# Optimization experiments

Measured on AMD Instinct MI355X. Metric: run time of the kernel, lower is better.

Reference implementation:

```python
import jax, jax.numpy as jnp
import numpy as np

BN_EPS = 1e-5  # torch BatchNorm1d default


def setup_inputs() -> dict:
    key = jax.random.key(0)
    k = jax.random.split(key, 5)
    B, D, L = 4096, 4096, 4  # batch, width, num layers (3 hidden + 1 output)
    x = jax.random.normal(k[0], (B, D), dtype=jnp.float32)
    # Per-layer Linear weights stored as [L, in, out]; scaled like xavier-ish init.
    W = jax.random.normal(k[1], (L, D, D), dtype=jnp.float32) * (1.0 / np.sqrt(D))
    b = jax.random.normal(k[2], (L, D), dtype=jnp.float32) * 0.01
    gamma = jax.random.uniform(k[3], (L, D), dtype=jnp.float32, minval=0.5, maxval=1.5)
    beta = jax.random.normal(k[4], (L, D), dtype=jnp.float32) * 0.1
    return {"x": x, "W": W, "b": b, "gamma": gamma, "beta": beta}


def _layer(h, W_l, b_l, gamma_l, beta_l):
    # one big GEMM replaces the per-neuron GEMV loop + stack
    h = h @ W_l + b_l  # [B, out]
    # BatchNorm1d, training mode: biased batch stats over the batch dim
    mu = jnp.mean(h, axis=0)
    var = jnp.var(h, axis=0)
    h = (h - mu) * jax.lax.rsqrt(var + BN_EPS) * gamma_l + beta_l
    return jax.nn.relu(h)


def reference(x, W, b, gamma, beta):
    out = x
    for l in range(W.shape[0]):  # small fixed layer count
        out = _layer(out, W[l], b[l], gamma[l], beta[l])
    # nn.Softmax(dim=0): softmax over the batch dimension, as in the original
    return jax.nn.softmax(out, axis=0)
```

## Files before the change

kernel.cpp:

```cpp
#include <hip/hip_runtime.h>
#include <stdint.h>

#define DIMD 4096
#define DIMB 4096
#define NLAYER 4
#define NT (DIMD / 64)

typedef unsigned short u16;
typedef __attribute__((ext_vector_type(4))) float f32x4;
typedef __attribute__((ext_vector_type(8))) __bf16 bf16x8;

__device__ __forceinline__ u16 f2bf(float f) {
    union { float f; uint32_t u; } v; v.f = f;
    return (u16)((v.u + 0x7fffu + ((v.u >> 16) & 1u)) >> 16);
}
__device__ __forceinline__ float bf2f(u16 u) {
    union { uint32_t u; float f; } v; v.u = ((uint32_t)u) << 16;
    return v.f;
}

__global__ void k_cvt(const float* __restrict__ in, u16* __restrict__ out) {
    int i = (blockIdx.x * 256 + threadIdx.x) * 4;
    float4 v = *reinterpret_cast<const float4*>(in + i);
    ushort4 r;
    r.x = f2bf(v.x); r.y = f2bf(v.y); r.z = f2bf(v.z); r.w = f2bf(v.w);
    *reinterpret_cast<ushort4*>(out + i) = r;
}

__global__ void k_trans(const float* __restrict__ W, u16* __restrict__ Wt) {
    __shared__ float tile[64][65];
    const int t = threadIdx.x;
    const size_t loff = (size_t)blockIdx.z * DIMD * DIMD;
    const int n0 = blockIdx.x * 64, k0 = blockIdx.y * 64;
    const int kr = t >> 4, c4 = (t & 15) * 4;
    #pragma unroll
    for (int r = 0; r < 4; ++r) {
        float4 v = *reinterpret_cast<const float4*>(W + loff + (size_t)(k0 + kr + r * 16) * DIMD + n0 + c4);
        tile[kr + r * 16][c4 + 0] = v.x;
        tile[kr + r * 16][c4 + 1] = v.y;
        tile[kr + r * 16][c4 + 2] = v.z;
        tile[kr + r * 16][c4 + 3] = v.w;
    }
    __syncthreads();
    const int nr = t >> 4, k4 = (t & 15) * 4;
    #pragma unroll
    for (int r = 0; r < 4; ++r) {
        int n = nr + r * 16;
        ushort4 o;
        o.x = f2bf(tile[k4 + 0][n]);
        o.y = f2bf(tile[k4 + 1][n]);
        o.z = f2bf(tile[k4 + 2][n]);
        o.w = f2bf(tile[k4 + 3][n]);
        *reinterpret_cast<ushort4*>(Wt + loff + (size_t)(n0 + n) * DIMD + k0 + k4) = o;
    }
}

#define GLD(g, l) __builtin_amdgcn_global_load_lds( \
    (__attribute__((address_space(1))) void*)(g),   \
    (__attribute__((address_space(3))) void*)(l), 16, 0, 0)

#define VMW8 asm volatile("s_waitcnt vmcnt(8)" ::: "memory")
#define VMW0 asm volatile("s_waitcnt vmcnt(0)" ::: "memory")
#define LGKM0 asm volatile("s_waitcnt lgkmcnt(0)" ::: "memory")

__global__ __launch_bounds__(512, 2) void k_gemm(
        const u16* __restrict__ A, const u16* __restrict__ Bt,
        const float* __restrict__ bias, u16* __restrict__ H,
        float* __restrict__ Hf,
        float* __restrict__ csum, float* __restrict__ csum2) {
    __shared__ __attribute__((aligned(16))) u16 As[2 * 256 * 64];
    __shared__ __attribute__((aligned(16))) u16 Bs[2 * 256 * 64];
    const int tid = threadIdx.x;
    const int lane = tid & 63, wv = tid >> 6;
    const int wm = wv >> 2, wn = wv & 3;
    const int bm = blockIdx.y, bn = blockIdx.x;
    const int lr = lane & 15, lk = lane >> 4;

    const int r0 = tid >> 3;
    const int cswz = (tid & 7) ^ (r0 & 7);
    const u16* gA = A  + (size_t)(bm * 256 + r0) * DIMD + cswz * 8;
    const u16* gB = Bt + (size_t)(bn * 256 + r0) * DIMD + cswz * 8;

#define STAGE_A(h, t, buf) do { \
    const u16* _s = gA + (size_t)(h) * 128 * DIMD + (size_t)(t) * 64; \
    u16* _d = As + (buf) * 16384 + (h) * 8192 + wv * 512; \
    GLD(_s, _d); GLD(_s + (size_t)64 * DIMD, _d + 4096); \
} while (0)
#define STAGE_B(h, t, buf) do { \
    const u16* _s = gB + (size_t)(h) * 128 * DIMD + (size_t)(t) * 64; \
    u16* _d = Bs + (buf) * 16384 + (h) * 8192 + wv * 512; \
    GLD(_s, _d); GLD(_s + (size_t)64 * DIMD, _d + 4096); \
} while (0)

    int aoff[4][2], boff[2][2];
    #pragma unroll
    for (int mf = 0; mf < 4; ++mf)
        #pragma unroll
        for (int ks = 0; ks < 2; ++ks) {
            int row = wm * 128 + mf * 16 + lr;
            aoff[mf][ks] = row * 64 + ((ks * 4 + lk) ^ (row & 7)) * 8;
        }
    #pragma unroll
    for (int nf = 0; nf < 2; ++nf)
        #pragma unroll
        for (int ks = 0; ks < 2; ++ks) {
            int row = wn * 64 + nf * 16 + lr;
            boff[nf][ks] = row * 64 + ((ks * 4 + lk) ^ (row & 7)) * 8;
        }

    f32x4 acc[8][4] = {};
    bf16x8 a[4][2], b0[2][2], b1[2][2];

#define READ_ALO(Ab) _Pragma("unroll") for (int mf = 0; mf < 4; ++mf) \
    _Pragma("unroll") for (int ks = 0; ks < 2; ++ks) \
        a[mf][ks] = *reinterpret_cast<const bf16x8*>((Ab) + aoff[mf][ks])
#define READ_AHI(Ab) _Pragma("unroll") for (int mf = 0; mf < 4; ++mf) \
    _Pragma("unroll") for (int ks = 0; ks < 2; ++ks) \
        a[mf][ks] = *reinterpret_cast<const bf16x8*>((Ab) + 4096 + aoff[mf][ks])
#define READ_B0(Bb) _Pragma("unroll") for (int nf = 0; nf < 2; ++nf) \
    _Pragma("unroll") for (int ks = 0; ks < 2; ++ks) \
        b0[nf][ks] = *reinterpret_cast<const bf16x8*>((Bb) + boff[nf][ks])
#define READ_B1(Bb) _Pragma("unroll") for (int nf = 0; nf < 2; ++nf) \
    _Pragma("unroll") for (int ks = 0; ks < 2; ++ks) \
        b1[nf][ks] = *reinterpret_cast<const bf16x8*>((Bb) + 2048 + boff[nf][ks])
#define MFMA_Q(MO, B, NO) _Pragma("unroll") for (int mf = 0; mf < 4; ++mf) \
    _Pragma("unroll") for (int nf = 0; nf < 2; ++nf) \
    _Pragma("unroll") for (int ks = 0; ks < 2; ++ks) \
        acc[(MO) + mf][(NO) + nf] = __builtin_amdgcn_mfma_f32_16x16x32_bf16( \
            a[mf][ks], B[nf][ks], acc[(MO) + mf][(NO) + nf], 0, 0, 0)

#define TILE(CUR, TN, PF, WEND) do { \
    const u16* Ab = As + (CUR) * 16384; \
    const u16* Bb = Bs + (CUR) * 16384; \
     \
    READ_ALO(Ab); READ_B0(Bb); \
    __builtin_amdgcn_s_barrier(); \
    LGKM0; \
    __builtin_amdgcn_s_setprio(1); \
    MFMA_Q(0, b0, 0); \
    __builtin_amdgcn_s_setprio(0); \
    __builtin_amdgcn_s_barrier(); \
     \
    READ_B1(Bb); \
    __builtin_amdgcn_s_barrier(); \
    LGKM0; \
    __builtin_amdgcn_s_setprio(1); \
    MFMA_Q(0, b1, 2); \
    __builtin_amdgcn_s_setprio(0); \
    __builtin_amdgcn_s_barrier(); \
     \
    READ_AHI(Ab); \
    if (PF) { STAGE_B(0, TN, CUR); STAGE_B(1, TN, CUR); } \
    __builtin_amdgcn_s_barrier(); \
    LGKM0; \
    __builtin_amdgcn_s_setprio(1); \
    MFMA_Q(4, b1, 2); \
    __builtin_amdgcn_s_setprio(0); \
    __builtin_amdgcn_s_barrier(); \
     \
    if (PF) { STAGE_A(0, TN, CUR); STAGE_A(1, TN, CUR); } \
    __builtin_amdgcn_s_setprio(1); \
    MFMA_Q(4, b0, 0); \
    __builtin_amdgcn_s_setprio(0); \
    WEND; \
    __builtin_amdgcn_s_barrier(); \
} while (0)

    STAGE_B(0, 0, 0); STAGE_B(1, 0, 0); STAGE_A(0, 0, 0); STAGE_A(1, 0, 0);
    STAGE_B(0, 1, 1); STAGE_B(1, 1, 1); STAGE_A(0, 1, 1); STAGE_A(1, 1, 1);
    VMW8;
    __builtin_amdgcn_s_barrier();

    for (int tt = 0; tt < NT - 2; tt += 2) {
        TILE(0, tt + 2, true, VMW8);
        TILE(1, tt + 3, true, VMW8);
    }
    TILE(0, 0, false, VMW0);
    TILE(1, 0, false, VMW0);

    #pragma unroll
    for (int nh = 0; nh < 2; ++nh)
        #pragma unroll
        for (int nf = 0; nf < 2; ++nf) {
            int n = nh * 2 + nf;
            int col = bn * 256 + wn * 64 + nh * 32 + nf * 16 + lr;
            float bv = bias[col];
            float s1 = 0.f, s2 = 0.f;
            #pragma unroll
            for (int m = 0; m < 8; ++m) {
                int rbase = bm * 256 + wm * 128 + (m >> 2) * 64 + (m & 3) * 16 + lk * 4;
                #pragma unroll
                for (int r = 0; r < 4; ++r) {
                    float v = acc[m][n][r] + bv;
                    if (Hf) Hf[(size_t)(rbase + r) * DIMD + col] = v;
                    else    H [(size_t)(rbase + r) * DIMD + col] = f2bf(v);
                    s1 += v; s2 += v * v;
                }
            }
            s1 += __shfl_xor(s1, 16); s1 += __shfl_xor(s1, 32);
            s2 += __shfl_xor(s2, 16); s2 += __shfl_xor(s2, 32);
            if (lk == 0) {
                atomicAdd(&csum[col], s1);
                atomicAdd(&csum2[col], s2);
            }
        }
#undef TILE
#undef STAGE_A
#undef STAGE_B
}

__global__ void k_norm(const u16* __restrict__ H, const float* __restrict__ sum,
                       const float* __restrict__ sum2, const float* __restrict__ gamma,
                       const float* __restrict__ beta, u16* __restrict__ o) {
    int j = (blockIdx.x * 256 + threadIdx.x) * 4;
    int i0 = blockIdx.y * 32;
    float4 sm = *reinterpret_cast<const float4*>(sum + j);
    float4 s2 = *reinterpret_cast<const float4*>(sum2 + j);
    float4 gm = *reinterpret_cast<const float4*>(gamma + j);
    float4 bt = *reinterpret_cast<const float4*>(beta + j);
    float s[4], tt[4];
    #pragma unroll
    for (int c = 0; c < 4; ++c) {
        float mu = (&sm.x)[c] * (1.0f / DIMB);
        float var = (&s2.x)[c] * (1.0f / DIMB) - mu * mu;
        s[c] = (&gm.x)[c] * rsqrtf(var + 1e-5f);
        tt[c] = (&bt.x)[c] - mu * s[c];
    }
    for (int i = i0; i < i0 + 32; ++i) {
        ushort4 h = *reinterpret_cast<const ushort4*>(H + (size_t)i * DIMD + j);
        ushort4 r;
        #pragma unroll
        for (int c = 0; c < 4; ++c)
            (&r.x)[c] = f2bf(fmaxf(bf2f((&h.x)[c]) * s[c] + tt[c], 0.0f));
        *reinterpret_cast<ushort4*>(o + (size_t)i * DIMD + j) = r;
    }
}

__global__ void k_esum(const float* __restrict__ H, const float* __restrict__ sum,
                       const float* __restrict__ sum2, const float* __restrict__ gamma,
                       const float* __restrict__ beta, float* __restrict__ esum) {
    int j = (blockIdx.x * 256 + threadIdx.x) * 4;
    int i0 = blockIdx.y * 32;
    float4 sm = *reinterpret_cast<const float4*>(sum + j);
    float4 s2 = *reinterpret_cast<const float4*>(sum2 + j);
    float4 gm = *reinterpret_cast<const float4*>(gamma + j);
    float4 bt = *reinterpret_cast<const float4*>(beta + j);
    float s[4], tt[4], acc[4] = {0.f, 0.f, 0.f, 0.f};
    #pragma unroll
    for (int c = 0; c < 4; ++c) {
        float mu = (&sm.x)[c] * (1.0f / DIMB);
        float var = (&s2.x)[c] * (1.0f / DIMB) - mu * mu;
        s[c] = (&gm.x)[c] * rsqrtf(var + 1e-5f);
        tt[c] = (&bt.x)[c] - mu * s[c];
    }
    for (int i = i0; i < i0 + 32; ++i) {
        float4 h = *reinterpret_cast<const float4*>(H + (size_t)i * DIMD + j);
        #pragma unroll
        for (int c = 0; c < 4; ++c)
            acc[c] += __expf(fmaxf((&h.x)[c] * s[c] + tt[c], 0.0f));
    }
    #pragma unroll
    for (int c = 0; c < 4; ++c) atomicAdd(&esum[j + c], acc[c]);
}

__global__ void k_final(float* __restrict__ H, const float* __restrict__ sum,
                        const float* __restrict__ sum2, const float* __restrict__ gamma,
                        const float* __restrict__ beta, const float* __restrict__ esum) {
    int j = (blockIdx.x * 256 + threadIdx.x) * 4;
    int i0 = blockIdx.y * 32;
    float4 sm = *reinterpret_cast<const float4*>(sum + j);
    float4 s2 = *reinterpret_cast<const float4*>(sum2 + j);
    float4 gm = *reinterpret_cast<const float4*>(gamma + j);
    float4 bt = *reinterpret_cast<const float4*>(beta + j);
    float4 es = *reinterpret_cast<const float4*>(esum + j);
    float s[4], tt[4], inv[4];
    #pragma unroll
    for (int c = 0; c < 4; ++c) {
        float mu = (&sm.x)[c] * (1.0f / DIMB);
        float var = (&s2.x)[c] * (1.0f / DIMB) - mu * mu;
        s[c] = (&gm.x)[c] * rsqrtf(var + 1e-5f);
        tt[c] = (&bt.x)[c] - mu * s[c];
        inv[c] = 1.0f / (&es.x)[c];
    }
    for (int i = i0; i < i0 + 32; ++i) {
        float4 h = *reinterpret_cast<const float4*>(H + (size_t)i * DIMD + j);
        float4 o;
        #pragma unroll
        for (int c = 0; c < 4; ++c)
            (&o.x)[c] = __expf(fmaxf((&h.x)[c] * s[c] + tt[c], 0.0f)) * inv[c];
        *reinterpret_cast<float4*>(H + (size_t)i * DIMD + j) = o;
    }
}

extern "C" void kernel_launch(void* const* d_in, const int* in_sizes, int n_in,
                              void* d_out, int out_size, void* d_ws, size_t ws_size,
                              hipStream_t stream) {
    (void)in_sizes; (void)n_in; (void)out_size; (void)ws_size;
    const float* x     = (const float*)d_in[0];
    const float* W     = (const float*)d_in[1];
    const float* b     = (const float*)d_in[2];
    const float* gamma = (const float*)d_in[3];
    const float* beta  = (const float*)d_in[4];
    float* out = (float*)d_out;

    char* ws = (char*)d_ws;
    u16*  Abf = (u16*)ws;
    u16*  Wt4 = (u16*)(ws + (size_t)32 * 1024 * 1024);
    u16*  Hbf = (u16*)(ws + (size_t)160 * 1024 * 1024);
    float* stats = (float*)(ws + (size_t)192 * 1024 * 1024);
    hipMemsetAsync(stats, 0, (4 * 8192 + 4096) * sizeof(float), stream);

    k_cvt<<<DIMB * DIMD / 1024, 256, 0, stream>>>(x, Abf);
    k_trans<<<dim3(64, 64, 4), 256, 0, stream>>>(W, Wt4);

    for (int l = 0; l < NLAYER; ++l) {
        float* sum = stats + l * 8192;
        float* sum2 = sum + 4096;
        float* Hf = (l == NLAYER - 1) ? out : nullptr;
        k_gemm<<<dim3(16, 16), 512, 0, stream>>>(Abf, Wt4 + (size_t)l * DIMD * DIMD,
                                                 b + l * DIMD, Hbf, Hf, sum, sum2);
        if (l < NLAYER - 1)
            k_norm<<<dim3(4, 128), 256, 0, stream>>>(Hbf, sum, sum2,
                gamma + l * DIMD, beta + l * DIMD, Abf);
    }
    k_esum<<<dim3(4, 128), 256, 0, stream>>>(out, stats + 3 * 8192, stats + 3 * 8192 + 4096,
        gamma + 3 * DIMD, beta + 3 * DIMD, stats + 32768);
    k_final<<<dim3(4, 128), 256, 0, stream>>>(out, stats + 3 * 8192, stats + 3 * 8192 + 4096,
        gamma + 3 * DIMD, beta + 3 * DIMD, stats + 32768);
}
```

Baseline: 708.0 us.

## Stage GEMM epilogue through LDS for coalesced vector stores; widen norm kernel

```diff
diff --git a/kernel.cpp b/kernel.cpp
--- a/kernel.cpp
+++ b/kernel.cpp
@@ -7,6 +7,7 @@
 #define NT (DIMD / 64)
 
 typedef unsigned short u16;
+typedef __attribute__((ext_vector_type(8))) unsigned short us8;
 typedef __attribute__((ext_vector_type(4))) float f32x4;
 typedef __attribute__((ext_vector_type(8))) __bf16 bf16x8;
 
@@ -132,7 +133,6 @@
 #define TILE(CUR, TN, PF, WEND) do { \
     const u16* Ab = As + (CUR) * 16384; \
     const u16* Bb = Bs + (CUR) * 16384; \
-     \
     READ_ALO(Ab); READ_B0(Bb); \
     __builtin_amdgcn_s_barrier(); \
     LGKM0; \
@@ -140,7 +140,6 @@
     MFMA_Q(0, b0, 0); \
     __builtin_amdgcn_s_setprio(0); \
     __builtin_amdgcn_s_barrier(); \
-     \
     READ_B1(Bb); \
     __builtin_amdgcn_s_barrier(); \
     LGKM0; \
@@ -148,7 +147,6 @@
     MFMA_Q(0, b1, 2); \
     __builtin_amdgcn_s_setprio(0); \
     __builtin_amdgcn_s_barrier(); \
-     \
     READ_AHI(Ab); \
     if (PF) { STAGE_B(0, TN, CUR); STAGE_B(1, TN, CUR); } \
     __builtin_amdgcn_s_barrier(); \
@@ -157,7 +155,6 @@
     MFMA_Q(4, b1, 2); \
     __builtin_amdgcn_s_setprio(0); \
     __builtin_amdgcn_s_barrier(); \
-     \
     if (PF) { STAGE_A(0, TN, CUR); STAGE_A(1, TN, CUR); } \
     __builtin_amdgcn_s_setprio(1); \
     MFMA_Q(4, b0, 0); \
@@ -183,20 +180,17 @@
         #pragma unroll
         for (int nf = 0; nf < 2; ++nf) {
             int n = nh * 2 + nf;
-            int col = bn * 256 + wn * 64 + nh * 32 + nf * 16 + lr;
+            int col = bn * 256 + wn * 64 + n * 16 + lr;
             float bv = bias[col];
             float s1 = 0.f, s2 = 0.f;
             #pragma unroll
-            for (int m = 0; m < 8; ++m) {
-                int rbase = bm * 256 + wm * 128 + (m >> 2) * 64 + (m & 3) * 16 + lk * 4;
+            for (int m = 0; m < 8; ++m)
                 #pragma unroll
                 for (int r = 0; r < 4; ++r) {
                     float v = acc[m][n][r] + bv;
-                    if (Hf) Hf[(size_t)(rbase + r) * DIMD + col] = v;
-                    else    H [(size_t)(rbase + r) * DIMD + col] = f2bf(v);
+                    acc[m][n][r] = v;
                     s1 += v; s2 += v * v;
                 }
-            }
             s1 += __shfl_xor(s1, 16); s1 += __shfl_xor(s1, 32);
             s2 += __shfl_xor(s2, 16); s2 += __shfl_xor(s2, 32);
             if (lk == 0) {
@@ -204,6 +198,38 @@
                 atomicAdd(&csum2[col], s2);
             }
         }
+
+    float* Ls = reinterpret_cast<float*>(As) + wv * 1088;
+    const int erow = lane >> 3, ecol = (lane & 7) * 8;
+    #pragma unroll
+    for (int mf = 0; mf < 8; ++mf) {
+        #pragma unroll
+        for (int n = 0; n < 4; ++n)
+            #pragma unroll
+            for (int r = 0; r < 4; ++r)
+                Ls[(lk * 4 + r) * 68 + n * 16 + lr] = acc[mf][n][r];
+        LGKM0;
+        #pragma unroll
+        for (int g = 0; g < 2; ++g) {
+            int rowloc = erow + g * 8;
+            size_t gidx = (size_t)(bm * 256 + wm * 128 + mf * 16 + rowloc) * DIMD
+                        + bn * 256 + wn * 64 + ecol;
+            const float* src = Ls + rowloc * 68 + ecol;
+            if (Hf) {
+                float4 v0, v1;
+                v0.x = src[0]; v0.y = src[1]; v0.z = src[2]; v0.w = src[3];
+                v1.x = src[4]; v1.y = src[5]; v1.z = src[6]; v1.w = src[7];
+                *reinterpret_cast<float4*>(Hf + gidx) = v0;
+                *reinterpret_cast<float4*>(Hf + gidx + 4) = v1;
+            } else {
+                us8 o;
+                #pragma unroll
+                for (int c = 0; c < 8; ++c) o[c] = f2bf(src[c]);
+                *reinterpret_cast<us8*>(H + gidx) = o;
+            }
+        }
+        LGKM0;
+    }
 #undef TILE
 #undef STAGE_A
 #undef STAGE_B
@@ -212,27 +238,30 @@
 __global__ void k_norm(const u16* __restrict__ H, const float* __restrict__ sum,
                        const float* __restrict__ sum2, const float* __restrict__ gamma,
                        const float* __restrict__ beta, u16* __restrict__ o) {
-    int j = (blockIdx.x * 256 + threadIdx.x) * 4;
+    int j = (blockIdx.x * 256 + threadIdx.x) * 8;
     int i0 = blockIdx.y * 32;
-    float4 sm = *reinterpret_cast<const float4*>(sum + j);
-    float4 s2 = *reinterpret_cast<const float4*>(sum2 + j);
-    float4 gm = *reinterpret_cast<const float4*>(gamma + j);
-    float4 bt = *reinterpret_cast<const float4*>(beta + j);
-    float s[4], tt[4];
-    #pragma unroll
-    for (int c = 0; c < 4; ++c) {
-        float mu = (&sm.x)[c] * (1.0f / DIMB);
-        float var = (&s2.x)[c] * (1.0f / DIMB) - mu * mu;
-        s[c] = (&gm.x)[c] * rsqrtf(var + 1e-5f);
-        tt[c] = (&bt.x)[c] - mu * s[c];
+    float s[8], tt[8];
+    #pragma unroll
+    for (int q = 0; q < 2; ++q) {
+        float4 sm = *reinterpret_cast<const float4*>(sum + j + q * 4);
+        float4 s2 = *reinterpret_cast<const float4*>(sum2 + j + q * 4);
+        float4 gm = *reinterpret_cast<const float4*>(gamma + j + q * 4);
+        float4 bt = *reinterpret_cast<const float4*>(beta + j + q * 4);
+        #pragma unroll
+        for (int c = 0; c < 4; ++c) {
+            float mu = (&sm.x)[c] * (1.0f / DIMB);
+            float var = (&s2.x)[c] * (1.0f / DIMB) - mu * mu;
+            s[q * 4 + c] = (&gm.x)[c] * rsqrtf(var + 1e-5f);
+            tt[q * 4 + c] = (&bt.x)[c] - mu * s[q * 4 + c];
+        }
     }
     for (int i = i0; i < i0 + 32; ++i) {
-        ushort4 h = *reinterpret_cast<const ushort4*>(H + (size_t)i * DIMD + j);
-        ushort4 r;
-        #pragma unroll
-        for (int c = 0; c < 4; ++c)
-            (&r.x)[c] = f2bf(fmaxf(bf2f((&h.x)[c]) * s[c] + tt[c], 0.0f));
-        *reinterpret_cast<ushort4*>(o + (size_t)i * DIMD + j) = r;
+        us8 h = *reinterpret_cast<const us8*>(H + (size_t)i * DIMD + j);
+        us8 r;
+        #pragma unroll
+        for (int c = 0; c < 8; ++c)
+            r[c] = f2bf(fmaxf(bf2f(h[c]) * s[c] + tt[c], 0.0f));
+        *reinterpret_cast<us8*>(o + (size_t)i * DIMD + j) = r;
     }
 }
 
@@ -320,7 +349,7 @@
         k_gemm<<<dim3(16, 16), 512, 0, stream>>>(Abf, Wt4 + (size_t)l * DIMD * DIMD,
                                                  b + l * DIMD, Hbf, Hf, sum, sum2);
         if (l < NLAYER - 1)
-            k_norm<<<dim3(4, 128), 256, 0, stream>>>(Hbf, sum, sum2,
+            k_norm<<<dim3(2, 128), 256, 0, stream>>>(Hbf, sum, sum2,
                 gamma + l * DIMD, beta + l * DIMD, Abf);
     }
     k_esum<<<dim3(4, 128), 256, 0, stream>>>(out, stats + 3 * 8192, stats + 3 * 8192 + 4096,
```

Result: faster. 682.0 us (-3.7%).
